# Performance work log

Measured on AMD Instinct MI355X. Metric: run time of the kernel, lower is better.

## Reference

```python
import jax, jax.numpy as jnp
import numpy as np

D_MODEL = 1024
MAX_ELEMENTS = 128


def setup_inputs() -> dict:
    key = jax.random.key(0)
    ks = jax.random.split(key, 12)
    B, S = 256, 128
    d, dq = D_MODEL, D_MODEL // 4
    inp = {
        "element_types": jax.random.randint(ks[0], (B, S), 0, 5, dtype=jnp.int64 if jax.config.jax_enable_x64 else jnp.int32),
        "element_indices": jax.random.randint(ks[1], (B, S), 0, MAX_ELEMENTS, dtype=jnp.int64 if jax.config.jax_enable_x64 else jnp.int32),
        "style_vectors": jax.random.normal(ks[2], (B, 5), dtype=jnp.float32),
        "page_captions": jax.random.normal(ks[3], (B, 768), dtype=jnp.float32),
        # learned parameters (torch Linear stored as [in, out] so y = x @ W + b)
        "type_emb": jax.random.normal(ks[4], (5, d), dtype=jnp.float32) * 0.02,
        "pos_emb": jax.random.normal(ks[5], (MAX_ELEMENTS, d), dtype=jnp.float32) * 0.02,
        "style_w1": jax.random.normal(ks[6], (5, dq), dtype=jnp.float32) * 0.02,
        "style_b1": jnp.zeros((dq,), dtype=jnp.float32),
        "style_w2": jax.random.normal(ks[7], (dq, d), dtype=jnp.float32) * 0.02,
        "style_b2": jnp.zeros((d,), dtype=jnp.float32),
        "text_w": jax.random.normal(ks[8], (768, d), dtype=jnp.float32) * 0.02,
        "text_b": jnp.zeros((d,), dtype=jnp.float32),
        "final_pos_emb": jax.random.normal(ks[9], (MAX_ELEMENTS, d), dtype=jnp.float32) * 0.02,
    }
    return inp


def reference(element_types, element_indices, style_vectors, page_captions,
              type_emb, pos_emb, style_w1, style_b1, style_w2, style_b2,
              text_w, text_b, final_pos_emb):
    B, S = element_types.shape
    # table gathers: [B, S, d]
    emb = type_emb[element_types] + pos_emb[element_indices]
    # per-batch style/text embeds computed ONCE (the torch loop recomputes them per step)
    style_embed = jnp.maximum(style_vectors @ style_w1 + style_b1, 0.0) @ style_w2 + style_b2  # [B, d]
    page_embed = page_captions @ text_w + text_b  # [B, d]
    # loop over i with mask (types[:, i] == 1) == broadcast masked add
    mask1 = (element_types == 1)[:, :, None]  # [B, S, 1]
    emb = emb + mask1 * (style_embed + page_embed)[:, None, :]
    # final positional encoding over positions 0..S-1
    emb = emb + final_pos_emb[:S][None, :, :]
    padding_mask = element_types == 0
    return emb, padding_mask
```

## Files before the change

### kernel.cpp

```cpp
#include <hip/hip_runtime.h>

#define D      1024
#define SEQ    128
#define BATCH  256
#define DQ     256
#define TEXTC  768

typedef float f32x4 __attribute__((ext_vector_type(4)));
typedef float f32x2 __attribute__((ext_vector_type(2)));

__global__ __launch_bounds__(256) void gemm_fused(
    const float* __restrict__ style_vectors,
    const float* __restrict__ page_captions,
    const float* __restrict__ style_w1,
    const float* __restrict__ style_b1,
    const float* __restrict__ style_w2,
    const float* __restrict__ style_b2,
    const float* __restrict__ text_w,
    const float* __restrict__ text_b,
    float* __restrict__ part)
{
    __shared__ float As[32][36];
    __shared__ float Bs[32][68];

    const int m0  = blockIdx.x * 32;
    const int n0  = blockIdx.y * 64;
    const int z   = blockIdx.z;
    const int tid = threadIdx.x;
    const int tm  = tid >> 4;
    const int tn  = tid & 15;

    const int am = tid >> 3;
    const int ak = (tid & 7) * 4;

    float sv[5];
    if (z == 0) {
#pragma unroll
        for (int j = 0; j < 5; ++j) sv[j] = style_vectors[(m0 + am) * 5 + j];
    }

    float acc[2][4] = {};

    for (int kc = 0; kc < 256; kc += 32) {
        if (z == 0) {
            int k = kc + ak;
#pragma unroll
            for (int r = 0; r < 4; ++r) {
                float h = style_b1[k + r];
#pragma unroll
                for (int j = 0; j < 5; ++j)
                    h = fmaf(sv[j], style_w1[j * DQ + k + r], h);
                As[ak + r][am] = fmaxf(h, 0.0f);
            }
        } else {
            float4 av = *(const float4*)
                &page_captions[(m0 + am) * TEXTC + (z * 256 - DQ) + kc + ak];
            As[ak + 0][am] = av.x;
            As[ak + 1][am] = av.y;
            As[ak + 2][am] = av.z;
            As[ak + 3][am] = av.w;
        }
        {
            int kk = tid >> 4;
            int nq = (tid & 15) * 4;
#pragma unroll
            for (int h = 0; h < 2; ++h) {
                int kl   = kk + 16 * h;
                int krow = z * 256 + kc + kl;
                const float* Wrow = (z == 0) ? &style_w2[krow * D]
                                             : &text_w[(krow - DQ) * D];
                *(f32x4*)&Bs[kl][nq] = *(const f32x4*)&Wrow[n0 + nq];
            }
        }
        __syncthreads();

#pragma unroll
        for (int kk = 0; kk < 32; ++kk) {
            f32x2 a2 = *(const f32x2*)&As[kk][tm * 2];
            f32x4 b4 = *(const f32x4*)&Bs[kk][tn * 4];
#pragma unroll
            for (int ii = 0; ii < 2; ++ii)
#pragma unroll
                for (int jj = 0; jj < 4; ++jj)
                    acc[ii][jj] = fmaf(a2[ii], b4[jj], acc[ii][jj]);
        }
        __syncthreads();
    }

    float* dst = part + (size_t)z * BATCH * D;
    const int n = n0 + tn * 4;
#pragma unroll
    for (int ii = 0; ii < 2; ++ii) {
        int m = m0 + tm * 2 + ii;
        f32x4 v = {acc[ii][0], acc[ii][1], acc[ii][2], acc[ii][3]};
        if (z == 0) {
            v[0] += style_b2[n + 0] + text_b[n + 0];
            v[1] += style_b2[n + 1] + text_b[n + 1];
            v[2] += style_b2[n + 2] + text_b[n + 2];
            v[3] += style_b2[n + 3] + text_b[n + 3];
        }
        *(f32x4*)&dst[m * D + n] = v;
    }
}

__global__ __launch_bounds__(256) void scatter_kernel(
    const int* __restrict__ types,
    const int* __restrict__ indices,
    const float* __restrict__ type_emb,
    const float* __restrict__ pos_emb,
    const float* __restrict__ final_pos_emb,
    const float* __restrict__ part,
    float* __restrict__ out_emb,
    float* __restrict__ out_mask)
{
    const int tid  = threadIdx.x;
    const int wave = tid >> 6;
    const int lane = tid & 63;
    const int bs   = blockIdx.x * 4 + wave;
    const int b    = bs >> 7;
    const int s    = bs & 127;
    const int et   = types[bs];
    const int ei   = indices[bs];

    const f32x4* te = (const f32x4*)&type_emb[et * D];
    const f32x4* pe = (const f32x4*)&pos_emb[ei * D];
    const f32x4* fe = (const f32x4*)&final_pos_emb[s * D];
    f32x4* dst = (f32x4*)out_emb + (size_t)bs * 256;

    if (et == 1) {
        const int Q = BATCH * D / 4;
        const f32x4* pp = (const f32x4*)part + b * 256;
#pragma unroll
        for (int j = 0; j < 4; ++j) {
            int idx = lane + 64 * j;
            f32x4 v = te[idx] + pe[idx] + fe[idx]
                    + pp[idx] + pp[idx + Q] + pp[idx + 2 * Q] + pp[idx + 3 * Q];
            __builtin_nontemporal_store(v, &dst[idx]);
        }
    } else {
#pragma unroll
        for (int j = 0; j < 4; ++j) {
            int idx = lane + 64 * j;
            f32x4 v = te[idx] + pe[idx] + fe[idx];
            __builtin_nontemporal_store(v, &dst[idx]);
        }
    }

    if (lane == 0)
        out_mask[bs] = (et == 0) ? 1.0f : 0.0f;
}

extern "C" void kernel_launch(void* const* d_in, const int* in_sizes, int n_in,
                              void* d_out, int out_size, void* d_ws, size_t ws_size,
                              hipStream_t stream) {
    const int*   element_types   = (const int*)  d_in[0];
    const int*   element_indices = (const int*)  d_in[1];
    const float* style_vectors   = (const float*)d_in[2];
    const float* page_captions   = (const float*)d_in[3];
    const float* type_emb        = (const float*)d_in[4];
    const float* pos_emb         = (const float*)d_in[5];
    const float* style_w1        = (const float*)d_in[6];
    const float* style_b1        = (const float*)d_in[7];
    const float* style_w2        = (const float*)d_in[8];
    const float* style_b2        = (const float*)d_in[9];
    const float* text_w          = (const float*)d_in[10];
    const float* text_b          = (const float*)d_in[11];
    const float* final_pos_emb   = (const float*)d_in[12];

    float* part = (float*)d_ws;

    float* out_emb  = (float*)d_out;
    float* out_mask = (float*)d_out + BATCH * SEQ * D;

    gemm_fused<<<dim3(BATCH / 32, D / 64, 4), 256, 0, stream>>>(
        style_vectors, page_captions, style_w1, style_b1,
        style_w2, style_b2, text_w, text_b, part);

    scatter_kernel<<<BATCH * SEQ / 4, 256, 0, stream>>>(
        element_types, element_indices, type_emb, pos_emb, final_pos_emb,
        part, out_emb, out_mask);
}
```

Baseline: 199.3 us.

## Overlap GEMM with non-style row scatter and defer style rows to second kernel

The first kernel now splits each block by wave role. Two waves compute independent 16x64 GEMM tiles using only wave-level barriers, while the other two waves write the output rows whose type is not 1, plus the padding mask. The second kernel sums the four partial products once per batch into shared memory and writes only the type-1 rows. The aim is to hide the small GEMM behind most of the memory-bound output writes and to stop re-reading the partials for every row. The cost is a less balanced workload split and more complex indexing.

```diff
diff --git a/kernel.cpp b/kernel.cpp
--- a/kernel.cpp
+++ b/kernel.cpp
@@ -7,9 +7,13 @@
 #define TEXTC  768
 
 typedef float f32x4 __attribute__((ext_vector_type(4)));
-typedef float f32x2 __attribute__((ext_vector_type(2)));
-
-__global__ __launch_bounds__(256) void gemm_fused(
+
+__global__ __launch_bounds__(256) void k1_gemm_scatter(
+    const int* __restrict__ types,
+    const int* __restrict__ indices,
+    const float* __restrict__ type_emb,
+    const float* __restrict__ pos_emb,
+    const float* __restrict__ final_pos_emb,
     const float* __restrict__ style_vectors,
     const float* __restrict__ page_captions,
     const float* __restrict__ style_w1,
@@ -18,136 +22,176 @@
     const float* __restrict__ style_b2,
     const float* __restrict__ text_w,
     const float* __restrict__ text_b,
-    float* __restrict__ part)
+    float* __restrict__ part,
+    float* __restrict__ out_emb,
+    float* __restrict__ out_mask)
 {
-    __shared__ float As[32][36];
-    __shared__ float Bs[32][68];
-
-    const int m0  = blockIdx.x * 32;
-    const int n0  = blockIdx.y * 64;
-    const int z   = blockIdx.z;
-    const int tid = threadIdx.x;
-    const int tm  = tid >> 4;
-    const int tn  = tid & 15;
-
-    const int am = tid >> 3;
-    const int ak = (tid & 7) * 4;
-
-    float sv[5];
-    if (z == 0) {
-#pragma unroll
-        for (int j = 0; j < 5; ++j) sv[j] = style_vectors[(m0 + am) * 5 + j];
-    }
-
-    float acc[2][4] = {};
-
-    for (int kc = 0; kc < 256; kc += 32) {
+    __shared__ float As[2][32][20];
+    __shared__ float Bs[2][32][68];
+
+    const int tid  = threadIdx.x;
+    const int wave = tid >> 6;
+    const int lane = tid & 63;
+    const int bid  = blockIdx.x;
+
+    if (wave < 2) {
+        const int w   = bid * 2 + wave;
+        const int z   = w >> 8;
+        const int rem = w & 255;
+        const int m0  = (rem & 15) << 4;
+        const int n0  = (rem >> 4) << 6;
+
+        float (*A)[20] = As[wave];
+        float (*B)[68] = Bs[wave];
+
+        const int sm  = lane >> 2;
+        const int sk  = (lane & 3) << 3;
+        const int tm4 = (lane >> 4) << 2;
+        const int tn4 = (lane & 15) << 2;
+        const int bkl = lane >> 4;
+
+        float sv[5];
         if (z == 0) {
-            int k = kc + ak;
-#pragma unroll
-            for (int r = 0; r < 4; ++r) {
-                float h = style_b1[k + r];
-#pragma unroll
-                for (int j = 0; j < 5; ++j)
-                    h = fmaf(sv[j], style_w1[j * DQ + k + r], h);
-                As[ak + r][am] = fmaxf(h, 0.0f);
-            }
-        } else {
-            float4 av = *(const float4*)
-                &page_captions[(m0 + am) * TEXTC + (z * 256 - DQ) + kc + ak];
-            As[ak + 0][am] = av.x;
-            As[ak + 1][am] = av.y;
-            As[ak + 2][am] = av.z;
-            As[ak + 3][am] = av.w;
-        }
-        {
-            int kk = tid >> 4;
-            int nq = (tid & 15) * 4;
-#pragma unroll
-            for (int h = 0; h < 2; ++h) {
-                int kl   = kk + 16 * h;
-                int krow = z * 256 + kc + kl;
+#pragma unroll
+            for (int j = 0; j < 5; ++j) sv[j] = style_vectors[(m0 + sm) * 5 + j];
+        }
+
+        f32x4 acc[4] = {};
+
+        for (int kc = 0; kc < 256; kc += 32) {
+            if (z == 0) {
+                const int kg = kc + sk;
+                f32x4 h0 = *(const f32x4*)&style_b1[kg];
+                f32x4 h1 = *(const f32x4*)&style_b1[kg + 4];
+#pragma unroll
+                for (int j = 0; j < 5; ++j) {
+                    h0 += sv[j] * *(const f32x4*)&style_w1[j * DQ + kg];
+                    h1 += sv[j] * *(const f32x4*)&style_w1[j * DQ + kg + 4];
+                }
+#pragma unroll
+                for (int r = 0; r < 4; ++r) {
+                    A[sk + r][sm]     = fmaxf(h0[r], 0.0f);
+                    A[sk + 4 + r][sm] = fmaxf(h1[r], 0.0f);
+                }
+            } else {
+                const float* cap =
+                    &page_captions[(m0 + sm) * TEXTC + (z - 1) * 256 + kc + sk];
+                f32x4 a0 = *(const f32x4*)cap;
+                f32x4 a1 = *(const f32x4*)(cap + 4);
+#pragma unroll
+                for (int r = 0; r < 4; ++r) {
+                    A[sk + r][sm]     = a0[r];
+                    A[sk + 4 + r][sm] = a1[r];
+                }
+            }
+#pragma unroll
+            for (int h = 0; h < 8; ++h) {
+                int kl   = bkl + (h << 2);
+                int krow = (z << 8) + kc + kl;
                 const float* Wrow = (z == 0) ? &style_w2[krow * D]
                                              : &text_w[(krow - DQ) * D];
-                *(f32x4*)&Bs[kl][nq] = *(const f32x4*)&Wrow[n0 + nq];
-            }
-        }
-        __syncthreads();
-
-#pragma unroll
-        for (int kk = 0; kk < 32; ++kk) {
-            f32x2 a2 = *(const f32x2*)&As[kk][tm * 2];
-            f32x4 b4 = *(const f32x4*)&Bs[kk][tn * 4];
-#pragma unroll
-            for (int ii = 0; ii < 2; ++ii)
-#pragma unroll
-                for (int jj = 0; jj < 4; ++jj)
-                    acc[ii][jj] = fmaf(a2[ii], b4[jj], acc[ii][jj]);
-        }
-        __syncthreads();
-    }
-
-    float* dst = part + (size_t)z * BATCH * D;
-    const int n = n0 + tn * 4;
-#pragma unroll
-    for (int ii = 0; ii < 2; ++ii) {
-        int m = m0 + tm * 2 + ii;
-        f32x4 v = {acc[ii][0], acc[ii][1], acc[ii][2], acc[ii][3]};
-        if (z == 0) {
-            v[0] += style_b2[n + 0] + text_b[n + 0];
-            v[1] += style_b2[n + 1] + text_b[n + 1];
-            v[2] += style_b2[n + 2] + text_b[n + 2];
-            v[3] += style_b2[n + 3] + text_b[n + 3];
-        }
-        *(f32x4*)&dst[m * D + n] = v;
+                *(f32x4*)&B[kl][tn4] = *(const f32x4*)&Wrow[n0 + tn4];
+            }
+            __builtin_amdgcn_wave_barrier();
+#pragma unroll
+            for (int kk = 0; kk < 32; ++kk) {
+                f32x4 a4 = *(const f32x4*)&A[kk][tm4];
+                f32x4 b4 = *(const f32x4*)&B[kk][tn4];
+#pragma unroll
+                for (int r = 0; r < 4; ++r)
+                    acc[r] += a4[r] * b4;
+            }
+            __builtin_amdgcn_wave_barrier();
+        }
+
+        f32x4 bias = {};
+        if (z == 0)
+            bias = *(const f32x4*)&style_b2[n0 + tn4]
+                 + *(const f32x4*)&text_b[n0 + tn4];
+#pragma unroll
+        for (int r = 0; r < 4; ++r) {
+            int m = m0 + tm4 + r;
+            f32x4 v = acc[r];
+            if (z == 0) v += bias;
+            *(f32x4*)&part[((size_t)z * BATCH + m) * D + n0 + tn4] = v;
+        }
+    } else {
+        const int r0 = bid * 64 + ((wave - 2) << 5);
+        const int lr = lane & 31;
+        const int myet = types[r0 + lr];
+        const int myei = indices[r0 + lr];
+        if (lane < 32)
+            out_mask[r0 + lane] = (myet == 0) ? 1.0f : 0.0f;
+
+#pragma unroll 4
+        for (int r = 0; r < 32; ++r) {
+            const int et = __shfl(myet, r);
+            const int ei = __shfl(myei, r);
+            if (et == 1) continue;
+            const int bs = r0 + r;
+            const int s  = bs & 127;
+            const f32x4* te = (const f32x4*)&type_emb[et * D];
+            const f32x4* pe = (const f32x4*)&pos_emb[ei * D];
+            const f32x4* fe = (const f32x4*)&final_pos_emb[s * D];
+            f32x4* dst = (f32x4*)out_emb + (size_t)bs * 256;
+#pragma unroll
+            for (int j = 0; j < 4; ++j) {
+                int idx = lane + (j << 6);
+                f32x4 v = te[idx] + pe[idx] + fe[idx];
+                __builtin_nontemporal_store(v, &dst[idx]);
+            }
+        }
     }
 }
 
-__global__ __launch_bounds__(256) void scatter_kernel(
+__global__ __launch_bounds__(256) void k2_comb_scatter(
     const int* __restrict__ types,
     const int* __restrict__ indices,
     const float* __restrict__ type_emb,
     const float* __restrict__ pos_emb,
     const float* __restrict__ final_pos_emb,
     const float* __restrict__ part,
-    float* __restrict__ out_emb,
-    float* __restrict__ out_mask)
+    float* __restrict__ out_emb)
 {
-    const int tid  = threadIdx.x;
+    __shared__ f32x4 comb[256];
+
+    const int tid = threadIdx.x;
+    const int bid = blockIdx.x;
+    const int b   = bid >> 1;
+    const int sh  = (bid & 1) << 6;
+
+    {
+        const int Q = BATCH * D / 4;
+        const f32x4* p = (const f32x4*)part + b * 256 + tid;
+        comb[tid] = p[0] + p[Q] + p[2 * Q] + p[3 * Q];
+    }
+    __syncthreads();
+
     const int wave = tid >> 6;
     const int lane = tid & 63;
-    const int bs   = blockIdx.x * 4 + wave;
-    const int b    = bs >> 7;
-    const int s    = bs & 127;
-    const int et   = types[bs];
-    const int ei   = indices[bs];
-
-    const f32x4* te = (const f32x4*)&type_emb[et * D];
-    const f32x4* pe = (const f32x4*)&pos_emb[ei * D];
-    const f32x4* fe = (const f32x4*)&final_pos_emb[s * D];
-    f32x4* dst = (f32x4*)out_emb + (size_t)bs * 256;
-
-    if (et == 1) {
-        const int Q = BATCH * D / 4;
-        const f32x4* pp = (const f32x4*)part + b * 256;
+    const int s0   = sh + (wave << 4);
+    const int bs0  = (b << 7) + s0;
+    const int myet = types[bs0 + (lane & 15)];
+    const int myei = indices[bs0 + (lane & 15)];
+
+#pragma unroll 4
+    for (int r = 0; r < 16; ++r) {
+        const int et = __shfl(myet, r);
+        const int ei = __shfl(myei, r);
+        if (et != 1) continue;
+        const int bs = bs0 + r;
+        const int s  = s0 + r;
+        const f32x4* te = (const f32x4*)&type_emb[et * D];
+        const f32x4* pe = (const f32x4*)&pos_emb[ei * D];
+        const f32x4* fe = (const f32x4*)&final_pos_emb[s * D];
+        f32x4* dst = (f32x4*)out_emb + (size_t)bs * 256;
 #pragma unroll
         for (int j = 0; j < 4; ++j) {
-            int idx = lane + 64 * j;
-            f32x4 v = te[idx] + pe[idx] + fe[idx]
-                    + pp[idx] + pp[idx + Q] + pp[idx + 2 * Q] + pp[idx + 3 * Q];
+            int idx = lane + (j << 6);
+            f32x4 v = te[idx] + pe[idx] + fe[idx] + comb[idx];
             __builtin_nontemporal_store(v, &dst[idx]);
         }
-    } else {
-#pragma unroll
-        for (int j = 0; j < 4; ++j) {
-            int idx = lane + 64 * j;
-            f32x4 v = te[idx] + pe[idx] + fe[idx];
-            __builtin_nontemporal_store(v, &dst[idx]);
-        }
     }
-
-    if (lane == 0)
-        out_mask[bs] = (et == 0) ? 1.0f : 0.0f;
 }
 
 extern "C" void kernel_launch(void* const* d_in, const int* in_sizes, int n_in,
@@ -172,11 +216,13 @@
     float* out_emb  = (float*)d_out;
     float* out_mask = (float*)d_out + BATCH * SEQ * D;
 
-    gemm_fused<<<dim3(BATCH / 32, D / 64, 4), 256, 0, stream>>>(
+    k1_gemm_scatter<<<512, 256, 0, stream>>>(
+        element_types, element_indices, type_emb, pos_emb, final_pos_emb,
         style_vectors, page_captions, style_w1, style_b1,
-        style_w2, style_b2, text_w, text_b, part);
-
-    scatter_kernel<<<BATCH * SEQ / 4, 256, 0, stream>>>(
+        style_w2, style_b2, text_w, text_b,
+        part, out_emb, out_mask);
+
+    k2_comb_scatter<<<512, 256, 0, stream>>>(
         element_types, element_indices, type_emb, pos_emb, final_pos_emb,
-        part, out_emb, out_mask);
+        part, out_emb);
 }
```

New measurement: 192.9 us (median of 2 runs). 3.2% less time.
